# Kernel optimization log

Hardware: AMD Instinct MI355X
Metric: run time of the kernel (lower is better)

## Reference

```python
import jax, jax.numpy as jnp
import numpy as np

WS = 2048            # window_size
STEP = WS // 2       # hop = window_size // 2
NC = WS // 2 + 1     # rfft coeffs
NB = 4               # n_blocks


def _hann():
    # periodic hann window (torch.hann_window default)
    return 0.5 - 0.5 * jnp.cos(2.0 * jnp.pi * jnp.arange(WS) / WS)


def _block(x, transfer, gain):
    # x: (b, 1, time); transfer: (NC,); gain: scalar
    b, ch, time = x.shape
    frames = time // STEP
    padded = jnp.pad(x, ((0, 0), (0, 0), (0, STEP)))
    idx = jnp.arange(frames)[:, None] * STEP + jnp.arange(WS)[None, :]
    windowed = padded[:, :, idx]                       # (b, ch, F, WS)
    spec = jnp.fft.rfft(windowed, axis=-1)             # (b, ch, F, NC) complex
    spec_t = jnp.moveaxis(spec, 2, 0)                  # (F, b, ch, NC)
    tc = transfer.astype(spec.dtype)

    # linear recurrence: out_i = transfer * (spec_i + out_{i-1})
    def step_fn(carry, s):
        out = (s + carry) * tc
        return out, out

    _, outs = jax.lax.scan(step_fn, jnp.zeros_like(spec_t[0]), spec_t)
    wins = jnp.fft.irfft(outs, n=WS, axis=-1) * _hann()  # (F, b, ch, WS)
    wins = jnp.moveaxis(wins, 0, 2)                      # (b, ch, F, WS)
    # overlap-add with hop = WS/2: split each frame into two halves
    first = wins[..., :STEP].reshape(b, ch, frames * STEP)
    second = wins[..., STEP:].reshape(b, ch, frames * STEP)
    samples = (jnp.pad(first, ((0, 0), (0, 0), (0, STEP)))
               + jnp.pad(second, ((0, 0), (0, 0), (STEP, 0))))
    return jnp.tanh(samples * gain)[..., :time]


def setup_inputs() -> dict:
    key = jax.random.key(0)
    k_x, k_b, k_s, k_g = jax.random.split(key, 4)
    x = jax.random.normal(k_x, (32, 1, 262144), dtype=jnp.float32)
    # init_transfer: sparse resonances * scaling * pitch^2
    resonances = (jax.random.uniform(k_b, (NB, NC)) < 0.01).astype(jnp.float32)
    scaling = jax.random.uniform(k_s, (NB, NC), minval=0.9, maxval=0.998)
    pitch = jnp.linspace(1.0, 0.0, NC) ** 2
    transfers = resonances * scaling * pitch[None, :]
    gains = jax.random.uniform(k_g, (NB,), minval=10.0, maxval=200.0)
    mixer = jnp.zeros((NB + 1,), dtype=jnp.float32)
    return {"x": x, "transfers": transfers, "gains": gains, "mixer": mixer}


def reference(x, transfers, gains, mixer):
    outputs = [x]
    inp = x
    for i in range(NB):
        inp = _block(inp, transfers[i], gains[i])
        outputs.append(inp)
    stacked = jnp.stack(outputs, axis=-1)          # (b, 1, time, NB+1)
    mixer_values = jax.nn.softmax(mixer)
    return jnp.sum(stacked * mixer_values, axis=-1)
```

## Files before the change

### kernel.cpp

```cpp
#include <hip/hip_runtime.h>
#include <math.h>
#include <stdint.h>

#define NB   4
#define NC   1025
#define WSZ  2048
#define STEP 1024
#define FRM  256
#define BAT  32
#define TT   262144
#define KC   32
#define YPAD 68

#define RREV (1.0f / 2048.0f)

typedef float f2 __attribute__((ext_vector_type(2)));

__device__ __forceinline__ float tanh_fast(float z) {
    float e = __expf(2.0f * z);
    return 1.0f - 2.0f / (e + 1.0f);
}

__device__ __forceinline__ void cis_rev(int idx, float* c, float* s) {
    float rev = (float)(idx & 2047) * RREV;
    *c = __builtin_amdgcn_cosf(rev);
    *s = __builtin_amdgcn_sinf(rev);
}

__global__ __launch_bounds__(1024) void setup_kernel(
    const float* __restrict__ transfers, const float* __restrict__ mixer,
    int* __restrict__ counts, int* __restrict__ bins, float* __restrict__ tvals,
    float* __restrict__ wmix, float* __restrict__ hann, int kmax)
{
    int i = blockIdx.x, tid = threadIdx.x;
    __shared__ int wcnt[16], woff[16];
    if (i == 0) {
        float cc, ss; cis_rev(tid, &cc, &ss);
        hann[tid] = 0.5f - 0.5f * cc;
    }
    float tv = transfers[i * NC + tid];
    bool nz = (tv != 0.0f);
    unsigned long long mask = __ballot(nz);
    int lane = tid & 63, w = tid >> 6;
    int within = __popcll(mask & ((1ULL << lane) - 1ULL));
    if (lane == 0) wcnt[w] = __popcll(mask);
    __syncthreads();
    if (tid == 0) {
        int acc = 0;
        for (int q = 0; q < 16; ++q) { woff[q] = acc; acc += wcnt[q]; }
        float tvL = transfers[i * NC + 1024];
        if (tvL != 0.0f && acc < kmax) { bins[i * NC + acc] = 1024; tvals[i * NC + acc] = tvL; acc++; }
        counts[i] = (acc < kmax) ? acc : kmax;
        if (i == 0) {
            float m = mixer[0];
            for (int q = 1; q < 5; ++q) m = fmaxf(m, mixer[q]);
            float e[5], s = 0.f;
            for (int q = 0; q < 5; ++q) { e[q] = __expf(mixer[q] - m); s += e[q]; }
            for (int q = 0; q < 5; ++q) wmix[q] = e[q] / s;
        }
    }
    __syncthreads();
    if (nz) {
        int pos = woff[w] + within;
        if (pos < kmax) { bins[i * NC + pos] = tid; tvals[i * NC + pos] = tv; }
    }
}

__global__ __launch_bounds__(256) void table_kernel(
    const int* __restrict__ counts, const int* __restrict__ bins,
    float2* __restrict__ cisA, float2* __restrict__ cisB, int kmax)
{
    int i = blockIdx.x >> 2, c = blockIdx.x & 3;
    int K = counts[i];
    int tid = threadIdx.x;
    for (int j = c; j < K; j += 4) {
        int k = bins[i * NC + j];
        if (tid < 64) {
            float cc, ss; cis_rev(k * tid, &cc, &ss);
            cisA[((size_t)i * kmax + j) * 64 + tid] = make_float2(cc, ss);
        } else if (tid < 80) {
            int q = tid - 64;
            float cc, ss; cis_rev(k * 64 * q, &cc, &ss);
            cisB[((size_t)i * kmax + j) * 16 + q] = make_float2(cc, ss);
        }
    }
}

__device__ __forceinline__ void half_dft(
    const float xr[16], int K, const float2* __restrict__ cA,
    const float2* __restrict__ cB, float2* __restrict__ Hout, int lane, int w)
{
    for (int j = w; j < K; j += 8) {
        int j2 = j + 4;
        bool two = (j2 < K);
        float2 bA = cB[(size_t)j * 16 + 1];
        float2 bB = two ? cB[(size_t)j2 * 16 + 1] : bA;
        float2 wAl = cA[(size_t)j * 64 + lane];
        float2 wBl = two ? cA[(size_t)j2 * 64 + lane] : wAl;
        f2 Wr, Wi, nWi;
        Wr.x = bA.x; Wr.y = bB.x;
        Wi.x = -bA.y; Wi.y = -bB.y;
        nWi = -Wi;
        f2 hr = 0.f, hi = 0.f;
#pragma unroll
        for (int i = 15; i >= 0; --i) {
            f2 xx; xx.x = xr[i]; xx.y = xr[i];
            f2 tmp = nWi * hi + xx;
            f2 nr = Wr * hr + tmp;
            hi = Wi * hr + Wr * hi;
            hr = nr;
        }
        f2 wlc, wls;
        wlc.x = wAl.x; wlc.y = wBl.x;
        wls.x = wAl.y; wls.y = wBl.y;
        f2 re = hr * wlc + hi * wls;
        f2 im = hi * wlc - hr * wls;
        float reA = re.x, imA = im.x, reB = re.y, imB = im.y;
#pragma unroll
        for (int m = 32; m >= 1; m >>= 1) {
            reA += __shfl_xor(reA, m, 64);
            imA += __shfl_xor(imA, m, 64);
            reB += __shfl_xor(reB, m, 64);
            imB += __shfl_xor(imB, m, 64);
        }
        if (lane == 0) {
            Hout[j] = make_float2(reA, imA);
            if (two) Hout[j2] = make_float2(reB, imB);
        }
    }
}

__global__ __launch_bounds__(256, 8) void analysis_kernel(
    const float* __restrict__ x, const int* __restrict__ counts,
    const float2* __restrict__ cisA, const float2* __restrict__ cisB,
    float2* __restrict__ H, int iblk, int kmax)
{
    int wg = blockIdx.x;
    int b = wg >> 8, h = wg & 255;
    int tid = threadIdx.x;
    int lane = tid & 63, w = tid >> 6;
    int K = counts[iblk];
    const float* xb = x + (size_t)b * TT + (size_t)h * STEP;
    float xr[16];
#pragma unroll
    for (int i = 0; i < 16; ++i) xr[i] = xb[lane + (i << 6)];
    const float2* cA = cisA + (size_t)iblk * kmax * 64;
    const float2* cB = cisB + (size_t)iblk * kmax * 16;
    float2* Hout = H + (size_t)(b * FRM + h) * K;
    half_dft(xr, K, cA, cB, Hout, lane, w);
}

__global__ __launch_bounds__(256) void scan_kernel(
    float2* __restrict__ S, const int* __restrict__ counts,
    const int* __restrict__ bins, const float* __restrict__ tvals, int iblk)
{
    int K = counts[iblk];
    int wg = blockIdx.x;
    int b = wg & (BAT - 1), j0 = wg >> 5;
    int f = threadIdx.x;
    __shared__ f2 sha[FRM];
    __shared__ float shg[FRM];
    for (int j = j0; j < K; j += 32) {
        float t = tvals[iblk * NC + j];
        int k = bins[iblk * NC + j];
        float2* Sb = S + (size_t)b * FRM * K + j;
        float2 h1 = Sb[(size_t)f * K];
        float2 h2 = (f < FRM - 1) ? Sb[(size_t)(f + 1) * K] : make_float2(0.f, 0.f);
        float sgn = (k & 1) ? -t : t;
        f2 a;
        a.x = fmaf(sgn, h2.x, h1.x * t);
        a.y = fmaf(sgn, h2.y, h1.y * t);
        float g = t;
#pragma unroll
        for (int d = 1; d < FRM; d <<= 1) {
            sha[f] = a; shg[f] = g;
            __syncthreads();
            if (f >= d) {
                f2 gg; gg.x = g; gg.y = g;
                a = gg * sha[f - d] + a;
                g *= shg[f - d];
            }
            __syncthreads();
        }
        Sb[(size_t)f * K] = make_float2(a.x, a.y);
        __syncthreads();
    }
}

__device__ __forceinline__ void acc4(
    f2& q0, f2& q1, f2& q2, f2& q3, float4 e, float4 a0, float4 a1)
{
    f2 up; up.x = e.x; up.y = e.y;
    f2 vp; vp.x = e.z; vp.y = e.w;
    q0 = up * a0.x + q0; q0 = vp * a0.y + q0;
    q1 = up * a0.z + q1; q1 = vp * a0.w + q1;
    q2 = up * a1.x + q2; q2 = vp * a1.y + q2;
    q3 = up * a1.z + q3; q3 = vp * a1.w + q3;
}

__global__ __launch_bounds__(256, 4) void fused_synth_kernel(
    const float2* __restrict__ S, float2* __restrict__ H2,
    const float2* __restrict__ cisA, const float2* __restrict__ cisB,
    const int* __restrict__ counts, const int* __restrict__ bins,
    const float* __restrict__ gains, const float* __restrict__ wmix,
    const float* __restrict__ hann, const float* __restrict__ x,
    float* __restrict__ dout, int iblk, int do_an, int kmax)
{
    __shared__ float4 smem[1024];
    float4* rc = smem;
    float*  ystage = (float*)smem;
    float4* part = smem + 544;

    int wg = blockIdx.x;
    int b = wg >> 7, s0 = (wg & 127) << 1;
    int tid = threadIdx.x;
    int n1 = tid << 2;
    int q = tid >> 4;
    int m = (tid & 15) << 2;

    int K = counts[iblk];
    const int* bl = bins + iblk * NC;
    const float2* Ob = S + (size_t)b * FRM * K;
    const float2* cA0 = cisA + (size_t)iblk * kmax * 64;
    const float2* cB0 = cisB + (size_t)iblk * kmax * 16;

    size_t base0 = (size_t)b * TT + ((size_t)s0 << 10) + (size_t)n1;
    const float* prevsrc = (iblk == 0) ? x : dout;
    float4 pv0 = *(const float4*)(prevsrc + base0);
    float4 pv1 = *(const float4*)(prevsrc + base0 + 1024);
    float4 hv = *(const float4*)(hann + n1);
    float gain = gains[iblk];
    float wsel = (iblk == 0) ? wmix[0] : 1.0f;
    float wn = wmix[iblk + 1];

    f2 p0 = 0.f, p1 = 0.f, p2 = 0.f, p3 = 0.f;
    f2 r0 = 0.f, r1 = 0.f, r2 = 0.f, r3 = 0.f;

    for (int c0 = 0; c0 < K; c0 += KC) {
        int cs = (K - c0 < KC) ? (K - c0) : KC;
        {
            int flat = tid >> 2;
            int seg = flat >> 5;
            int j = flat & 31;
            int jj = c0 + ((j < cs) ? j : (cs - 1));
            int q0 = (tid & 3) << 2;
            int k = bl[jj];
            float g = ((k == 0) || (k == 1024)) ? (1.0f / 2048.0f) : (2.0f / 2048.0f);
            float sg = (k & 1) ? -g : g;
            int fc = s0 + seg;
            float2 o1 = Ob[(size_t)fc * K + jj];
            float2 om = (fc > 0) ? Ob[(size_t)(fc - 1) * K + jj] : make_float2(0.f, 0.f);
            float c2r = om.x * sg, c2i = om.y * sg;
            f2 u; u.x = c2r;  u.y = o1.x * g - c2r;
            f2 v; v.x = -c2i; v.y = -(o1.y * g - c2i);
            const float2* bqp = cB0 + (size_t)jj * 16 + q0;
#pragma unroll
            for (int e = 0; e < 4; ++e) {
                float2 bq = bqp[e];
                f2 up = u * bq.x + v * bq.y;
                f2 vp = v * bq.x - u * bq.y;
                rc[(flat << 4) + q0 + e] = make_float4(up.x, up.y, vp.x, vp.y);
            }
        }
        __syncthreads();
        const float2* cAj = cA0 + ((size_t)c0 << 6) + m;
        const float4* rcq = rc + q;
        int jj = 0;
        for (; jj + 2 <= cs; jj += 2) {
            float4 a00 = *(const float4*)(cAj);
            float4 a01 = *(const float4*)(cAj + 2);
            float4 a10 = *(const float4*)(cAj + 64);
            float4 a11 = *(const float4*)(cAj + 66);
            cAj += 128;
            float4 e00 = rcq[jj << 4];
            float4 e01 = rcq[(KC + jj) << 4];
            float4 e10 = rcq[(jj + 1) << 4];
            float4 e11 = rcq[(KC + jj + 1) << 4];
            acc4(p0, p1, p2, p3, e00, a00, a01);
            acc4(r0, r1, r2, r3, e01, a00, a01);
            acc4(p0, p1, p2, p3, e10, a10, a11);
            acc4(r0, r1, r2, r3, e11, a10, a11);
        }
        if (jj < cs) {
            float4 a0 = *(const float4*)(cAj);
            float4 a1 = *(const float4*)(cAj + 2);
            float4 e0 = rcq[jj << 4];
            float4 e1 = rcq[(KC + jj) << 4];
            acc4(p0, p1, p2, p3, e0, a0, a1);
            acc4(r0, r1, r2, r3, e1, a0, a1);
        }
        __syncthreads();
    }

    float4 yv0, yv1;
    yv0.x = tanh_fast(fmaf(hv.x, p0.y, p0.x) * gain);
    yv0.y = tanh_fast(fmaf(hv.y, p1.y, p1.x) * gain);
    yv0.z = tanh_fast(fmaf(hv.z, p2.y, p2.x) * gain);
    yv0.w = tanh_fast(fmaf(hv.w, p3.y, p3.x) * gain);
    yv1.x = tanh_fast(fmaf(hv.x, r0.y, r0.x) * gain);
    yv1.y = tanh_fast(fmaf(hv.y, r1.y, r1.x) * gain);
    yv1.z = tanh_fast(fmaf(hv.z, r2.y, r2.x) * gain);
    yv1.w = tanh_fast(fmaf(hv.w, r3.y, r3.x) * gain);

    float4 dv0, dv1;
    dv0.x = fmaf(wsel, pv0.x, wn * yv0.x);
    dv0.y = fmaf(wsel, pv0.y, wn * yv0.y);
    dv0.z = fmaf(wsel, pv0.z, wn * yv0.z);
    dv0.w = fmaf(wsel, pv0.w, wn * yv0.w);
    dv1.x = fmaf(wsel, pv1.x, wn * yv1.x);
    dv1.y = fmaf(wsel, pv1.y, wn * yv1.y);
    dv1.z = fmaf(wsel, pv1.z, wn * yv1.z);
    dv1.w = fmaf(wsel, pv1.w, wn * yv1.w);
    *(float4*)(dout + base0) = dv0;
    *(float4*)(dout + base0 + 1024) = dv1;

    if (do_an) {
        int cw = n1 >> 6, off = n1 & 63;
        *(float4*)(ystage + cw * YPAD + off) = yv0;
        *(float4*)(ystage + 16 * YPAD + cw * YPAD + off) = yv1;
        __syncthreads();
        int K2 = counts[iblk + 1];
        if (K2 > 0) {
            const float2* cA2 = cisA + (size_t)(iblk + 1) * kmax * 64;
            const float2* cB2 = cisB + (size_t)(iblk + 1) * kmax * 16;
            int jloc = tid & 15, c = tid >> 4;
            const float4* yp0 = (const float4*)(ystage + c * YPAD);
            const float4* yp1 = (const float4*)(ystage + 16 * YPAD + c * YPAD);
            for (int jb = 0; jb < K2; jb += 16) {
                int j = jb + jloc;
                int js = (j < K2) ? j : (K2 - 1);
                float2 w1 = cA2[(size_t)js * 64 + 1];
                float Wr = w1.x, Wi = -w1.y, nWi = w1.y;
                f2 hr = 0.f, hi = 0.f;
#pragma unroll
                for (int i4 = 15; i4 >= 0; --i4) {
                    float4 ya = yp0[i4];
                    float4 yb = yp1[i4];
                    { f2 yy; yy.x = ya.w; yy.y = yb.w;
                      f2 t = hi * nWi + yy; f2 nr = hr * Wr + t; hi = hr * Wi + hi * Wr; hr = nr; }
                    { f2 yy; yy.x = ya.z; yy.y = yb.z;
                      f2 t = hi * nWi + yy; f2 nr = hr * Wr + t; hi = hr * Wi + hi * Wr; hr = nr; }
                    { f2 yy; yy.x = ya.y; yy.y = yb.y;
                      f2 t = hi * nWi + yy; f2 nr = hr * Wr + t; hi = hr * Wi + hi * Wr; hr = nr; }
                    { f2 yy; yy.x = ya.x; yy.y = yb.x;
                      f2 t = hi * nWi + yy; f2 nr = hr * Wr + t; hi = hr * Wi + hi * Wr; hr = nr; }
                }
                float2 bq = cB2[(size_t)js * 16 + c];
                f2 re = hr * bq.x + hi * bq.y;
                f2 im = hi * bq.x - hr * bq.y;
                part[c * 16 + jloc] = make_float4(re.x, im.x, re.y, im.y);
                __syncthreads();
                if (tid < 16) {
                    int j2 = jb + tid;
                    if (j2 < K2) {
                        float4 acc = part[tid];
                        for (int cc = 1; cc < 16; ++cc) {
                            float4 pp = part[cc * 16 + tid];
                            acc.x += pp.x; acc.y += pp.y; acc.z += pp.z; acc.w += pp.w;
                        }
                        H2[(size_t)(b * FRM + s0) * K2 + j2] = make_float2(acc.x, acc.y);
                        H2[(size_t)(b * FRM + s0 + 1) * K2 + j2] = make_float2(acc.z, acc.w);
                    }
                }
                __syncthreads();
            }
        }
    }
}

extern "C" void kernel_launch(void* const* d_in, const int* in_sizes, int n_in,
                              void* d_out, int out_size, void* d_ws, size_t ws_size,
                              hipStream_t stream)
{
    const float* x         = (const float*)d_in[0];
    const float* transfers = (const float*)d_in[1];
    const float* gains     = (const float*)d_in[2];
    const float* mixer     = (const float*)d_in[3];
    float* dout = (float*)d_out;

    uint8_t* ws = (uint8_t*)d_ws;
    int*   counts = (int*)ws;
    int*   bins   = (int*)(ws + 64);
    float* tvals  = (float*)(ws + 64 + 16400);
    float* wmix   = (float*)(ws + 64 + 16400 + 16400);
    float* hann   = (float*)(ws + 36864);
    const size_t HDR = 65536;

    long long perk = 2LL * BAT * FRM * 8 + (long long)NB * 80 * 8;
    long long km = ((long long)ws_size - (long long)HDR) / perk;
    int kmax = (int)((km < 1) ? 1 : ((km > NC) ? NC : km));
    float2* S0 = (float2*)(ws + HDR);
    float2* S1 = S0 + (size_t)BAT * FRM * kmax;
    float2* cisA = S1 + (size_t)BAT * FRM * kmax;
    float2* cisB = cisA + (size_t)NB * kmax * 64;

    setup_kernel<<<NB, 1024, 0, stream>>>(transfers, mixer, counts, bins, tvals, wmix, hann, kmax);
    table_kernel<<<NB * 4, 256, 0, stream>>>(counts, bins, cisA, cisB, kmax);
    analysis_kernel<<<BAT * FRM, 256, 0, stream>>>(x, counts, cisA, cisB, S0, 0, kmax);

    float2* cur = S0;
    float2* nxt = S1;
    for (int i = 0; i < NB; ++i) {
        scan_kernel<<<BAT * 32, 256, 0, stream>>>(cur, counts, bins, tvals, i);
        fused_synth_kernel<<<BAT * 128, 256, 0, stream>>>(cur, nxt, cisA, cisB, counts, bins,
                                                          gains, wmix, hann, x, dout, i,
                                                          (i < NB - 1) ? 1 : 0, kmax);
        float2* t = cur; cur = nxt; nxt = t;
    }
}
```

Baseline: 244.5 us.

## Use wavefront shuffles for scan and partial reductions, raise occupancy hint

Replaces the 8-step shared-memory Hillis-Steele scan over 256 frames with an in-wavefront shuffle scan, then a cross-wave carry fix-up that uses precomputed powers of the transfer coefficient. This cuts the barrier count per bin from 16 to 2. The analysis partial reduction now reduces across lanes with xor shuffles before a 4-way shared-memory sum, replacing a 16-way serial sum. It also raises the launch-bounds occupancy hint from 4 to 6 and moves the prev/hann/gain loads after the main loop to shorten register live ranges, which risks register spills.

```diff
diff --git a/kernel.cpp b/kernel.cpp
--- a/kernel.cpp
+++ b/kernel.cpp
@@ -158,8 +158,8 @@
     int wg = blockIdx.x;
     int b = wg & (BAT - 1), j0 = wg >> 5;
     int f = threadIdx.x;
-    __shared__ f2 sha[FRM];
-    __shared__ float shg[FRM];
+    int lane = f & 63, w = f >> 6;
+    __shared__ float2 wtot[4];
     for (int j = j0; j < K; j += 32) {
         float t = tvals[iblk * NC + j];
         int k = bins[iblk * NC + j];
@@ -167,22 +167,42 @@
         float2 h1 = Sb[(size_t)f * K];
         float2 h2 = (f < FRM - 1) ? Sb[(size_t)(f + 1) * K] : make_float2(0.f, 0.f);
         float sgn = (k & 1) ? -t : t;
-        f2 a;
-        a.x = fmaf(sgn, h2.x, h1.x * t);
-        a.y = fmaf(sgn, h2.y, h1.y * t);
-        float g = t;
-#pragma unroll
-        for (int d = 1; d < FRM; d <<= 1) {
-            sha[f] = a; shg[f] = g;
-            __syncthreads();
-            if (f >= d) {
-                f2 gg; gg.x = g; gg.y = g;
-                a = gg * sha[f - d] + a;
-                g *= shg[f - d];
+        float ax = fmaf(sgn, h2.x, h1.x * t);
+        float ay = fmaf(sgn, h2.y, h1.y * t);
+        float td = t;
+        float tp0, tp1, tp2, tp3, tp4, tp5;
+#pragma unroll
+        for (int s = 0; s < 6; ++s) {
+            int d = 1 << s;
+            if (s == 0) tp0 = td; else if (s == 1) tp1 = td; else if (s == 2) tp2 = td;
+            else if (s == 3) tp3 = td; else if (s == 4) tp4 = td; else tp5 = td;
+            float bx = __shfl_up(ax, d, 64);
+            float by = __shfl_up(ay, d, 64);
+            if (lane >= d) { ax = fmaf(td, bx, ax); ay = fmaf(td, by, ay); }
+            td *= td;
+        }
+        if (lane == 63) wtot[w] = make_float2(ax, ay);
+        __syncthreads();
+        float px = 0.f, py = 0.f;
+#pragma unroll
+        for (int w2 = 0; w2 < 3; ++w2) {
+            if (w2 < w) {
+                float2 v = wtot[w2];
+                px = fmaf(px, td, v.x);
+                py = fmaf(py, td, v.y);
             }
-            __syncthreads();
-        }
-        Sb[(size_t)f * K] = make_float2(a.x, a.y);
+        }
+        int n = lane + 1;
+        float fac = (n & 64) ? td : 1.0f;
+        if (n & 1)  fac *= tp0;
+        if (n & 2)  fac *= tp1;
+        if (n & 4)  fac *= tp2;
+        if (n & 8)  fac *= tp3;
+        if (n & 16) fac *= tp4;
+        if (n & 32) fac *= tp5;
+        ax = fmaf(fac, px, ax);
+        ay = fmaf(fac, py, ay);
+        Sb[(size_t)f * K] = make_float2(ax, ay);
         __syncthreads();
     }
 }
@@ -198,7 +218,7 @@
     q3 = up * a1.z + q3; q3 = vp * a1.w + q3;
 }
 
-__global__ __launch_bounds__(256, 4) void fused_synth_kernel(
+__global__ __launch_bounds__(256, 6) void fused_synth_kernel(
     const float2* __restrict__ S, float2* __restrict__ H2,
     const float2* __restrict__ cisA, const float2* __restrict__ cisB,
     const int* __restrict__ counts, const int* __restrict__ bins,
@@ -223,15 +243,6 @@
     const float2* Ob = S + (size_t)b * FRM * K;
     const float2* cA0 = cisA + (size_t)iblk * kmax * 64;
     const float2* cB0 = cisB + (size_t)iblk * kmax * 16;
-
-    size_t base0 = (size_t)b * TT + ((size_t)s0 << 10) + (size_t)n1;
-    const float* prevsrc = (iblk == 0) ? x : dout;
-    float4 pv0 = *(const float4*)(prevsrc + base0);
-    float4 pv1 = *(const float4*)(prevsrc + base0 + 1024);
-    float4 hv = *(const float4*)(hann + n1);
-    float gain = gains[iblk];
-    float wsel = (iblk == 0) ? wmix[0] : 1.0f;
-    float wn = wmix[iblk + 1];
 
     f2 p0 = 0.f, p1 = 0.f, p2 = 0.f, p3 = 0.f;
     f2 r0 = 0.f, r1 = 0.f, r2 = 0.f, r3 = 0.f;
@@ -292,6 +303,15 @@
         __syncthreads();
     }
 
+    size_t base0 = (size_t)b * TT + ((size_t)s0 << 10) + (size_t)n1;
+    const float* prevsrc = (iblk == 0) ? x : dout;
+    float4 pv0 = *(const float4*)(prevsrc + base0);
+    float4 pv1 = *(const float4*)(prevsrc + base0 + 1024);
+    float4 hv = *(const float4*)(hann + n1);
+    float gain = gains[iblk];
+    float wsel = (iblk == 0) ? wmix[0] : 1.0f;
+    float wn = wmix[iblk + 1];
+
     float4 yv0, yv1;
     yv0.x = tanh_fast(fmaf(hv.x, p0.y, p0.x) * gain);
     yv0.y = tanh_fast(fmaf(hv.y, p1.y, p1.x) * gain);
@@ -324,6 +344,7 @@
             const float2* cA2 = cisA + (size_t)(iblk + 1) * kmax * 64;
             const float2* cB2 = cisB + (size_t)(iblk + 1) * kmax * 16;
             int jloc = tid & 15, c = tid >> 4;
+            int lane = tid & 63, wv = tid >> 6;
             const float4* yp0 = (const float4*)(ystage + c * YPAD);
             const float4* yp1 = (const float4*)(ystage + 16 * YPAD + c * YPAD);
             for (int jb = 0; jb < K2; jb += 16) {
@@ -348,16 +369,29 @@
                 float2 bq = cB2[(size_t)js * 16 + c];
                 f2 re = hr * bq.x + hi * bq.y;
                 f2 im = hi * bq.x - hr * bq.y;
-                part[c * 16 + jloc] = make_float4(re.x, im.x, re.y, im.y);
+                float4 pr = make_float4(re.x, im.x, re.y, im.y);
+                pr.x += __shfl_xor(pr.x, 16, 64);
+                pr.y += __shfl_xor(pr.y, 16, 64);
+                pr.z += __shfl_xor(pr.z, 16, 64);
+                pr.w += __shfl_xor(pr.w, 16, 64);
+                pr.x += __shfl_xor(pr.x, 32, 64);
+                pr.y += __shfl_xor(pr.y, 32, 64);
+                pr.z += __shfl_xor(pr.z, 32, 64);
+                pr.w += __shfl_xor(pr.w, 32, 64);
+                if (lane < 16) part[wv * 16 + lane] = pr;
                 __syncthreads();
                 if (tid < 16) {
                     int j2 = jb + tid;
                     if (j2 < K2) {
-                        float4 acc = part[tid];
-                        for (int cc = 1; cc < 16; ++cc) {
-                            float4 pp = part[cc * 16 + tid];
-                            acc.x += pp.x; acc.y += pp.y; acc.z += pp.z; acc.w += pp.w;
-                        }
+                        float4 a0 = part[tid];
+                        float4 a1 = part[16 + tid];
+                        float4 a2 = part[32 + tid];
+                        float4 a3 = part[48 + tid];
+                        float4 acc;
+                        acc.x = (a0.x + a1.x) + (a2.x + a3.x);
+                        acc.y = (a0.y + a1.y) + (a2.y + a3.y);
+                        acc.z = (a0.z + a1.z) + (a2.z + a3.z);
+                        acc.w = (a0.w + a1.w) + (a2.w + a3.w);
                         H2[(size_t)(b * FRM + s0) * K2 + j2] = make_float2(acc.x, acc.y);
                         H2[(size_t)(b * FRM + s0 + 1) * K2 + j2] = make_float2(acc.z, acc.w);
                     }
```

Result: no change. 240.3 us (-1.7%).
